# Performance work log

Measured on AMD Instinct MI355X. Metric: run time of the kernel, lower is better.

## Reference

```python
import jax, jax.numpy as jnp
import numpy as np

N_HEAD = 12

def setup_inputs() -> dict:
    key = jax.random.key(0)
    k1, k2, k3 = jax.random.split(key, 3)
    B, T, C = 8, 1024, 768
    x = jax.random.normal(k1, (B, T, C), dtype=jnp.float32)
    # torch Linear(768, 3*768): store as [in, out] so we can do x @ W
    W_attn = jax.random.normal(k2, (C, 3 * C), dtype=jnp.float32) * 0.02
    b_attn = jax.random.normal(k3, (3 * C,), dtype=jnp.float32) * 0.02
    return {"x": x, "W_attn": W_attn, "b_attn": b_attn}

def reference(x, W_attn, b_attn):
    B, T, C = x.shape
    H = N_HEAD
    hs = C // H
    scale = 1.0 / jnp.sqrt(jnp.asarray(hs, dtype=x.dtype))
    qkv = x @ W_attn + b_attn                      # [B,T,3C]
    q, k, v = jnp.split(qkv, 3, axis=-1)
    q = q.reshape(B, T, H, hs).transpose(0, 2, 1, 3)  # [B,H,T,hs]
    k = k.reshape(B, T, H, hs).transpose(0, 2, 1, 3)
    v = v.reshape(B, T, H, hs).transpose(0, 2, 1, 3)
    scores = jnp.einsum('bhqd,bhkd->bhqk', q, k) * scale
    # causal mask then ReLU (masked -inf entries become 0 after ReLU)
    causal = jnp.tril(jnp.ones((T, T), dtype=bool))
    att = jnp.where(causal[None, None], jax.nn.relu(scores), jnp.zeros((), dtype=scores.dtype))
    out = jnp.einsum('bhqk,bhkd->bhqd', att, v)    # [B,H,T,hs]
    out = out.transpose(0, 2, 1, 3).reshape(B, T, C)
    return out
```

## Files before the change

kernel.cpp:

```cpp
#include <hip/hip_runtime.h>

typedef __attribute__((ext_vector_type(8))) short bf16x8;
typedef __attribute__((ext_vector_type(4))) short bf16x4;
typedef __attribute__((ext_vector_type(4))) float f32x4;
typedef __attribute__((ext_vector_type(4))) unsigned short us4;
typedef __attribute__((ext_vector_type(8))) unsigned short us8;

#define MFMA(a, b, c) __builtin_amdgcn_mfma_f32_16x16x32_bf16((a), (b), (c), 0, 0, 0)
#define MFMA16(a, b, c) __builtin_amdgcn_mfma_f32_16x16x16bf16_1k((a), (b), (c), 0, 0, 0)

__device__ __forceinline__ unsigned short f2bf(float f) {
  unsigned u = __builtin_bit_cast(unsigned, f);
  u = (u + 0x7fffu + ((u >> 16) & 1u)) >> 16;
  return (unsigned short)u;
}

__device__ __forceinline__ unsigned cvt_pk_bf16(float lo, float hi) {
  unsigned r;
  asm("v_cvt_pk_bf16_f32 %0, %1, %2" : "=v"(r) : "v"(lo), "v"(hi));
  return r;
}

__device__ __forceinline__ void gload16(const void* g, void* l) {
  __builtin_amdgcn_global_load_lds((const __attribute__((address_space(1))) void*)g,
                                   (__attribute__((address_space(3))) void*)l,
                                   16, 0, 0);
}

__device__ __forceinline__ bf16x8 readfrag(const unsigned short* buf, int row, int kbyte) {
  int byte = row * 128 + kbyte;
  byte ^= (row & 7) << 4;
  return *(const bf16x8*)((const char*)buf + byte);
}

__device__ __forceinline__ bf16x4 readfrag64(const unsigned short* buf, int row, int col) {
  int byte = (row * 128 + col * 2) ^ ((row & 7) << 4);
  return *(const bf16x4*)((const char*)buf + byte);
}

__global__ void cast_x_kernel(const float* __restrict__ x,
                              unsigned short* __restrict__ xb, int n4) {
  int id = blockIdx.x * blockDim.x + threadIdx.x;
  if (id >= n4) return;
  float4 v = ((const float4*)x)[id];
  us4 o = { f2bf(v.x), f2bf(v.y), f2bf(v.z), f2bf(v.w) };
  ((us4*)xb)[id] = o;
}

__global__ void castw_kernel(const float* __restrict__ W,
                             unsigned short* __restrict__ Wt) {
  __shared__ unsigned short tile[32][33];
  int bn = blockIdx.x * 32;
  int bk = blockIdx.y * 32;
  int lx = threadIdx.x & 31, ly = threadIdx.x >> 5;
#pragma unroll
  for (int i = 0; i < 32; i += 8)
    tile[ly + i][lx] = f2bf(W[(bk + ly + i) * 2304 + bn + lx]);
  __syncthreads();
#pragma unroll
  for (int i = 0; i < 32; i += 8)
    Wt[(bn + ly + i) * 768 + bk + lx] = tile[lx][ly + i];
}

__global__ __launch_bounds__(256, 2) void qkv_gemm_kernel(
    const unsigned short* __restrict__ xb, const unsigned short* __restrict__ wt,
    const float* __restrict__ bias,
    unsigned short* __restrict__ qb, unsigned short* __restrict__ kb,
    unsigned short* __restrict__ vb) {
  __shared__ unsigned short lds[40960];
  const int tid = threadIdx.x;
  const int lane = tid & 63, wid = tid >> 6;
  const int wm = wid >> 1, wn = wid & 1;
  const int l15 = lane & 15, lg = lane >> 4;

  int bid = blockIdx.x;
  int xcd = bid & 7, c = bid >> 3;
  int mb = xcd * 8 + (c & 7);
  int nb = c >> 3;
  const int m0 = mb * 128, n0 = nb * 128;

  const unsigned short* Ab_g = xb + (size_t)m0 * 768;
  const unsigned short* Bb_g = wt + (size_t)n0 * 768;

  int eA[4], sA[4];
#pragma unroll
  for (int i = 0; i < 4; ++i) {
    int e = (i * 256 + tid) * 8, row = e >> 6;
    eA[i] = e;
    sA[i] = row * 768 + ((e ^ ((row & 7) << 3)) & 63);
  }

#define SA(buf, k0, i) gload16(Ab_g + sA[i] + (k0), &lds[(buf) * 8192 + eA[i]])
#define SB(buf, k0, i) gload16(Bb_g + sA[i] + (k0), &lds[24576 + (buf) * 8192 + eA[i]])

  f32x4 acc[4][4] = {};
  bf16x8 bfr[4][2];

  SA(0, 0, 0); SA(0, 0, 1); SA(0, 0, 2); SA(0, 0, 3);
  SB(0, 0, 0); SB(0, 0, 1); SB(0, 0, 2); SB(0, 0, 3);
  SA(1, 64, 0); SA(1, 64, 1); SA(1, 64, 2); SA(1, 64, 3);
  asm volatile("s_waitcnt vmcnt(4)" ::: "memory");
  __builtin_amdgcn_s_barrier();

#define GPHASE(cA_, cB_, P, STG, EW)                                              \
  {                                                                               \
    const unsigned short* Abuf = &lds[(cA_) * 8192];                              \
    const unsigned short* Bbuf = &lds[24576 + (cB_) * 8192];                      \
    bf16x8 afr[2][2];                                                             \
    _Pragma("unroll") for (int m2 = 0; m2 < 2; ++m2)                              \
        _Pragma("unroll") for (int kk = 0; kk < 2; ++kk)                          \
            afr[m2][kk] =                                                         \
        readfrag(Abuf, wm * 64 + ((P) * 2 + m2) * 16 + l15, kk * 64 + lg * 16);   \
    if ((P) == 0) {                                                               \
      _Pragma("unroll") for (int nf = 0; nf < 4; ++nf)                            \
          _Pragma("unroll") for (int kk = 0; kk < 2; ++kk)                        \
              bfr[nf][kk] =                                                       \
          readfrag(Bbuf, wn * 64 + nf * 16 + l15, kk * 64 + lg * 16);             \
    }                                                                             \
    STG;                                                                          \
    __builtin_amdgcn_sched_barrier(0);                                            \
    __builtin_amdgcn_s_barrier();                                                 \
    asm volatile("s_waitcnt lgkmcnt(0)" ::: "memory");                            \
    __builtin_amdgcn_sched_barrier(0);                                            \
    __builtin_amdgcn_s_setprio(1);                                                \
    _Pragma("unroll") for (int m2 = 0; m2 < 2; ++m2)                              \
        _Pragma("unroll") for (int nf = 0; nf < 4; ++nf)                          \
            _Pragma("unroll") for (int kk = 0; kk < 2; ++kk)                      \
                acc[(P) * 2 + m2][nf] =                                           \
        MFMA(afr[m2][kk], bfr[nf][kk], acc[(P) * 2 + m2][nf]);                    \
    __builtin_amdgcn_s_setprio(0);                                                \
    EW;                                                                           \
    __builtin_amdgcn_sched_barrier(0);                                            \
    __builtin_amdgcn_s_barrier();                                                 \
  }

  int cA = 0;
  for (int t = 0; t < 10; ++t) {
    int cB = t & 1, cBn = cB ^ 1;
    int cA2 = cA + 2; if (cA2 >= 3) cA2 -= 3;
    int k1 = (t + 1) * 64, k2 = (t + 2) * 64;
    GPHASE(cA, cB, 0, { SB(cBn, k1, 0); SB(cBn, k1, 1); SB(cBn, k1, 2); SB(cBn, k1, 3); }, );
    GPHASE(cA, cB, 1, { SA(cA2, k2, 0); SA(cA2, k2, 1); SA(cA2, k2, 2); SA(cA2, k2, 3); },
           asm volatile("s_waitcnt vmcnt(4)" ::: "memory"));
    cA = (cA == 2) ? 0 : cA + 1;
  }
  GPHASE(cA, 0, 0, { SB(1, 704, 0); SB(1, 704, 1); SB(1, 704, 2); SB(1, 704, 3); }, );
  GPHASE(cA, 0, 1, , asm volatile("s_waitcnt vmcnt(0)" ::: "memory"));
  cA = (cA == 2) ? 0 : cA + 1;
  GPHASE(cA, 1, 0, , );
  GPHASE(cA, 1, 1, , );

  __syncthreads();

  const int sec = n0 / 768;
  const float qscale = (sec == 0) ? 0.125f : 1.0f;
  float bcol[4];
#pragma unroll
  for (int nf = 0; nf < 4; ++nf) bcol[nf] = bias[n0 + wn * 64 + nf * 16 + l15];

  if (sec < 2) {
    unsigned short* ct = lds;
#pragma unroll
    for (int mf = 0; mf < 4; ++mf)
#pragma unroll
      for (int nf = 0; nf < 4; ++nf)
#pragma unroll
        for (int r = 0; r < 4; ++r)
          ct[(wm * 64 + mf * 16 + lg * 4 + r) * 128 + wn * 64 + nf * 16 + l15] =
              f2bf((acc[mf][nf][r] + bcol[nf]) * qscale);
    __syncthreads();
    unsigned short* dstbase = (sec == 0) ? qb : kb;
    const int hbase = (n0 - sec * 768) >> 6;
    const int g8 = tid >> 3, l8 = tid & 7;
#pragma unroll
    for (int j = 0; j < 8; ++j) {
      int chunk = j * 32 + g8;
      int row = chunk >> 1, hh = chunk & 1;
      us8 v = *(const us8*)&ct[row * 128 + hh * 64 + l8 * 8];
      int t = m0 + row, bb = t >> 10, tt = t & 1023;
      *(us8*)(dstbase + ((size_t)((bb * 12 + hbase + hh) * 1024 + tt)) * 64 + l8 * 8) = v;
    }
  } else {
#pragma unroll
    for (int nf = 0; nf < 4; ++nf) {
      int cc2 = (n0 - 1536) + wn * 64 + nf * 16 + l15;
      int h = cc2 >> 6, d = cc2 & 63;
#pragma unroll
      for (int mf = 0; mf < 4; ++mf) {
        int row0 = m0 + wm * 64 + mf * 16 + lg * 4;
        int bb = row0 >> 10, t0 = row0 & 1023;
        us4 o;
#pragma unroll
        for (int r = 0; r < 4; ++r) o[r] = f2bf(acc[mf][nf][r] + bcol[nf]);
        *(us4*)(vb + ((size_t)((bb * 12 + h) * 64 + d)) * 1024 + t0) = o;
      }
    }
  }
#undef SA
#undef SB
#undef GPHASE
}

__global__ __launch_bounds__(512, 2) void attn_kernel(
    const unsigned short* __restrict__ qb, const unsigned short* __restrict__ kb,
    const unsigned short* __restrict__ vb, float* __restrict__ out) {
  __shared__ unsigned short lds[32768];
  const int tid = threadIdx.x;
  const int lane = tid & 63, wid = tid >> 6;
  const int qs = wid >> 1, ks = wid & 1;
  const int l15 = lane & 15, lg = lane >> 4;

  int bid = blockIdx.x;
  int xcd = bid & 7, c = bid >> 3;
  int bh = xcd * 12 + (c % 12);
  int byq = 3 - (c / 12);
  const int b = bh / 12, h = bh % 12;
  const size_t base = (size_t)bh * 65536;
  const int Q = byq * 4 + qs;
  const int qr0 = byq * 256 + qs * 64;

  bf16x8 aq[4][2];
#pragma unroll
  for (int mf = 0; mf < 4; ++mf)
#pragma unroll
    for (int kk = 0; kk < 2; ++kk)
      aq[mf][kk] = *(const bf16x8*)(qb + base + (size_t)(qr0 + mf * 16 + l15) * 64 +
                                    kk * 32 + lg * 8);

  const int e = tid * 8;
  const int row = e >> 6;
  const int esw = e ^ ((row & 7) << 3);

#define ASTAGE(buf, i_)                                                            \
  {                                                                                \
    int kt0 = 2 * (i_);                                                            \
    gload16(kb + base + (size_t)kt0 * 4096 + esw, &lds[(buf) * 8192 + e]);         \
    gload16(kb + base + (size_t)(kt0 + 1) * 4096 + esw,                            \
            &lds[(buf) * 8192 + 4096 + e]);                                        \
    gload16(vb + base + (size_t)row * 1024 + kt0 * 64 + (esw & 63),                \
            &lds[16384 + (buf) * 8192 + e]);                                       \
    gload16(vb + base + (size_t)row * 1024 + (kt0 + 1) * 64 + (esw & 63),          \
            &lds[16384 + (buf) * 8192 + 4096 + e]);                                \
  }

  f32x4 o[4][4] = {};

  const int niter = 2 * byq + 2;
  ASTAGE(0, 0);
  asm volatile("s_waitcnt vmcnt(0)" ::: "memory");
  __builtin_amdgcn_s_barrier();

  for (int i = 0; i < niter; ++i) {
    const int cur = i & 1;
    if (i + 1 < niter) ASTAGE(cur ^ 1, i + 1);
    const int kt = 2 * i + ks;
    if (kt <= Q) {
      const unsigned short* Kb = &lds[cur * 8192 + ks * 4096];
      const unsigned short* Vb = &lds[16384 + cur * 8192 + ks * 4096];
      bf16x8 bk[4][2];
#pragma unroll
      for (int nf = 0; nf < 4; ++nf)
#pragma unroll
        for (int kk = 0; kk < 2; ++kk)
          bk[nf][kk] = readfrag(Kb, nf * 16 + l15, kk * 64 + lg * 16);
      bf16x4 vf[4][4];
#pragma unroll
      for (int nf = 0; nf < 4; ++nf)
#pragma unroll
        for (int df = 0; df < 4; ++df)
          vf[nf][df] = readfrag64(Vb, df * 16 + l15, nf * 16 + lg * 4);
      const bool diag = (kt == Q);
      bf16x4 pa[4][4];
      __builtin_amdgcn_s_setprio(1);
#pragma unroll
      for (int mf = 0; mf < 4; ++mf)
#pragma unroll
        for (int nf = 0; nf < 4; ++nf) {
          f32x4 s = {};
          s = MFMA(bk[nf][0], aq[mf][0], s);
          s = MFMA(bk[nf][1], aq[mf][1], s);
          float v0, v1, v2, v3;
          if (diag) {
            int q = mf * 16 + l15, k0 = nf * 16 + lg * 4;
            v0 = (k0 + 0 <= q) ? fmaxf(s[0], 0.0f) : 0.0f;
            v1 = (k0 + 1 <= q) ? fmaxf(s[1], 0.0f) : 0.0f;
            v2 = (k0 + 2 <= q) ? fmaxf(s[2], 0.0f) : 0.0f;
            v3 = (k0 + 3 <= q) ? fmaxf(s[3], 0.0f) : 0.0f;
          } else {
            v0 = fmaxf(s[0], 0.0f);
            v1 = fmaxf(s[1], 0.0f);
            v2 = fmaxf(s[2], 0.0f);
            v3 = fmaxf(s[3], 0.0f);
          }
          uint2 w;
          w.x = cvt_pk_bf16(v0, v1);
          w.y = cvt_pk_bf16(v2, v3);
          pa[mf][nf] = __builtin_bit_cast(bf16x4, w);
        }
#pragma unroll
      for (int nf = 0; nf < 4; ++nf)
#pragma unroll
        for (int mf = 0; mf < 4; ++mf)
#pragma unroll
          for (int df = 0; df < 4; ++df)
            o[mf][df] = MFMA16(pa[mf][nf], vf[nf][df], o[mf][df]);
      __builtin_amdgcn_s_setprio(0);
    }
    asm volatile("s_waitcnt vmcnt(0)" ::: "memory");
    __builtin_amdgcn_sched_barrier(0);
    __builtin_amdgcn_s_barrier();
  }
#undef ASTAGE

  float* fr = (float*)lds;
  if (ks == 1) {
#pragma unroll
    for (int mf = 0; mf < 4; ++mf)
#pragma unroll
      for (int df = 0; df < 4; ++df)
#pragma unroll
        for (int r = 0; r < 4; ++r) {
          int rowq = mf * 16 + lg * 4 + r, col = df * 16 + l15;
          int idx = (qs * 4096 + rowq * 64 + col) ^ ((rowq & 4) << 2);
          fr[idx] = o[mf][df][r];
        }
  }
  __syncthreads();
  if (ks == 0) {
#pragma unroll
    for (int mf = 0; mf < 4; ++mf)
#pragma unroll
      for (int df = 0; df < 4; ++df)
#pragma unroll
        for (int r = 0; r < 4; ++r) {
          int rowq = mf * 16 + lg * 4 + r, col = df * 16 + l15;
          int idx = (qs * 4096 + rowq * 64 + col) ^ ((rowq & 4) << 2);
          float v = o[mf][df][r] + fr[idx];
          out[(size_t)(b * 1024 + qr0 + rowq) * 768 + h * 64 + col] = v;
        }
  }
}

extern "C" void kernel_launch(void* const* d_in, const int* in_sizes, int n_in,
                              void* d_out, int out_size, void* d_ws, size_t ws_size,
                              hipStream_t stream) {
  const float* x = (const float*)d_in[0];
  const float* W = (const float*)d_in[1];
  const float* bias = (const float*)d_in[2];
  float* out = (float*)d_out;

  unsigned short* xb = (unsigned short*)d_ws;
  unsigned short* wt = xb + 6291456;
  unsigned short* qb = wt + 1769472;
  unsigned short* kb = qb + 6291456;
  unsigned short* vb = kb + 6291456;

  cast_x_kernel<<<6144, 256, 0, stream>>>(x, xb, 1572864);
  castw_kernel<<<dim3(72, 24), 256, 0, stream>>>(W, wt);
  qkv_gemm_kernel<<<1152, 256, 0, stream>>>(xb, wt, bias, qb, kb, vb);
  attn_kernel<<<384, 512, 0, stream>>>(qb, kb, vb, out);
}
```

Baseline: 84.63 us.

## Replace pipelined QKV GEMM with single-buffered loop and higher occupancy

```diff
diff --git a/kernel.cpp b/kernel.cpp
--- a/kernel.cpp
+++ b/kernel.cpp
@@ -62,12 +62,12 @@
     Wt[(bn + ly + i) * 768 + bk + lx] = tile[lx][ly + i];
 }
 
-__global__ __launch_bounds__(256, 2) void qkv_gemm_kernel(
+__global__ __launch_bounds__(256, 4) void qkv_gemm_kernel(
     const unsigned short* __restrict__ xb, const unsigned short* __restrict__ wt,
     const float* __restrict__ bias,
     unsigned short* __restrict__ qb, unsigned short* __restrict__ kb,
     unsigned short* __restrict__ vb) {
-  __shared__ unsigned short lds[40960];
+  __shared__ unsigned short lds[16384];
   const int tid = threadIdx.x;
   const int lane = tid & 63, wid = tid >> 6;
   const int wm = wid >> 1, wn = wid & 1;
@@ -90,67 +90,38 @@
     sA[i] = row * 768 + ((e ^ ((row & 7) << 3)) & 63);
   }
 
-#define SA(buf, k0, i) gload16(Ab_g + sA[i] + (k0), &lds[(buf) * 8192 + eA[i]])
-#define SB(buf, k0, i) gload16(Bb_g + sA[i] + (k0), &lds[24576 + (buf) * 8192 + eA[i]])
-
   f32x4 acc[4][4] = {};
-  bf16x8 bfr[4][2];
-
-  SA(0, 0, 0); SA(0, 0, 1); SA(0, 0, 2); SA(0, 0, 3);
-  SB(0, 0, 0); SB(0, 0, 1); SB(0, 0, 2); SB(0, 0, 3);
-  SA(1, 64, 0); SA(1, 64, 1); SA(1, 64, 2); SA(1, 64, 3);
-  asm volatile("s_waitcnt vmcnt(4)" ::: "memory");
-  __builtin_amdgcn_s_barrier();
-
-#define GPHASE(cA_, cB_, P, STG, EW)                                              \
-  {                                                                               \
-    const unsigned short* Abuf = &lds[(cA_) * 8192];                              \
-    const unsigned short* Bbuf = &lds[24576 + (cB_) * 8192];                      \
-    bf16x8 afr[2][2];                                                             \
-    _Pragma("unroll") for (int m2 = 0; m2 < 2; ++m2)                              \
-        _Pragma("unroll") for (int kk = 0; kk < 2; ++kk)                          \
-            afr[m2][kk] =                                                         \
-        readfrag(Abuf, wm * 64 + ((P) * 2 + m2) * 16 + l15, kk * 64 + lg * 16);   \
-    if ((P) == 0) {                                                               \
-      _Pragma("unroll") for (int nf = 0; nf < 4; ++nf)                            \
-          _Pragma("unroll") for (int kk = 0; kk < 2; ++kk)                        \
-              bfr[nf][kk] =                                                       \
-          readfrag(Bbuf, wn * 64 + nf * 16 + l15, kk * 64 + lg * 16);             \
-    }                                                                             \
-    STG;                                                                          \
-    __builtin_amdgcn_sched_barrier(0);                                            \
-    __builtin_amdgcn_s_barrier();                                                 \
-    asm volatile("s_waitcnt lgkmcnt(0)" ::: "memory");                            \
-    __builtin_amdgcn_sched_barrier(0);                                            \
-    __builtin_amdgcn_s_setprio(1);                                                \
-    _Pragma("unroll") for (int m2 = 0; m2 < 2; ++m2)                              \
-        _Pragma("unroll") for (int nf = 0; nf < 4; ++nf)                          \
-            _Pragma("unroll") for (int kk = 0; kk < 2; ++kk)                      \
-                acc[(P) * 2 + m2][nf] =                                           \
-        MFMA(afr[m2][kk], bfr[nf][kk], acc[(P) * 2 + m2][nf]);                    \
-    __builtin_amdgcn_s_setprio(0);                                                \
-    EW;                                                                           \
-    __builtin_amdgcn_sched_barrier(0);                                            \
-    __builtin_amdgcn_s_barrier();                                                 \
-  }
-
-  int cA = 0;
-  for (int t = 0; t < 10; ++t) {
-    int cB = t & 1, cBn = cB ^ 1;
-    int cA2 = cA + 2; if (cA2 >= 3) cA2 -= 3;
-    int k1 = (t + 1) * 64, k2 = (t + 2) * 64;
-    GPHASE(cA, cB, 0, { SB(cBn, k1, 0); SB(cBn, k1, 1); SB(cBn, k1, 2); SB(cBn, k1, 3); }, );
-    GPHASE(cA, cB, 1, { SA(cA2, k2, 0); SA(cA2, k2, 1); SA(cA2, k2, 2); SA(cA2, k2, 3); },
-           asm volatile("s_waitcnt vmcnt(4)" ::: "memory"));
-    cA = (cA == 2) ? 0 : cA + 1;
-  }
-  GPHASE(cA, 0, 0, { SB(1, 704, 0); SB(1, 704, 1); SB(1, 704, 2); SB(1, 704, 3); }, );
-  GPHASE(cA, 0, 1, , asm volatile("s_waitcnt vmcnt(0)" ::: "memory"));
-  cA = (cA == 2) ? 0 : cA + 1;
-  GPHASE(cA, 1, 0, , );
-  GPHASE(cA, 1, 1, , );
-
-  __syncthreads();
+
+  for (int t = 0; t < 12; ++t) {
+    const int k0 = t * 64;
+#pragma unroll
+    for (int i = 0; i < 4; ++i) {
+      gload16(Ab_g + sA[i] + k0, &lds[eA[i]]);
+      gload16(Bb_g + sA[i] + k0, &lds[8192 + eA[i]]);
+    }
+    asm volatile("s_waitcnt vmcnt(0)" ::: "memory");
+    __syncthreads();
+
+    bf16x8 afr[4][2], bfr[4][2];
+#pragma unroll
+    for (int mf = 0; mf < 4; ++mf)
+#pragma unroll
+      for (int kk = 0; kk < 2; ++kk)
+        afr[mf][kk] = readfrag(lds, wm * 64 + mf * 16 + l15, kk * 64 + lg * 16);
+#pragma unroll
+    for (int nf = 0; nf < 4; ++nf)
+#pragma unroll
+      for (int kk = 0; kk < 2; ++kk)
+        bfr[nf][kk] = readfrag(&lds[8192], wn * 64 + nf * 16 + l15, kk * 64 + lg * 16);
+#pragma unroll
+    for (int mf = 0; mf < 4; ++mf)
+#pragma unroll
+      for (int nf = 0; nf < 4; ++nf)
+#pragma unroll
+        for (int kk = 0; kk < 2; ++kk)
+          acc[mf][nf] = MFMA(afr[mf][kk], bfr[nf][kk], acc[mf][nf]);
+    __syncthreads();
+  }
 
   const int sec = n0 / 768;
   const float qscale = (sec == 0) ? 0.125f : 1.0f;
@@ -196,9 +167,6 @@
       }
     }
   }
-#undef SA
-#undef SB
-#undef GPHASE
 }
 
 __global__ __launch_bounds__(512, 2) void attn_kernel(
```

Result: slower. 87.76 us (+3.7%).

## Merge two-phase GEMM k-step into single iteration with one barrier

Applied to the files above, without the earlier changes.

```diff
diff --git a/kernel.cpp b/kernel.cpp
--- a/kernel.cpp
+++ b/kernel.cpp
@@ -94,7 +94,6 @@
 #define SB(buf, k0, i) gload16(Bb_g + sA[i] + (k0), &lds[24576 + (buf) * 8192 + eA[i]])
 
   f32x4 acc[4][4] = {};
-  bf16x8 bfr[4][2];
 
   SA(0, 0, 0); SA(0, 0, 1); SA(0, 0, 2); SA(0, 0, 3);
   SB(0, 0, 0); SB(0, 0, 1); SB(0, 0, 2); SB(0, 0, 3);
@@ -102,35 +101,27 @@
   asm volatile("s_waitcnt vmcnt(4)" ::: "memory");
   __builtin_amdgcn_s_barrier();
 
-#define GPHASE(cA_, cB_, P, STG, EW)                                              \
+#define GITER(cA_, cB_, STG, EW)                                                  \
   {                                                                               \
     const unsigned short* Abuf = &lds[(cA_) * 8192];                              \
     const unsigned short* Bbuf = &lds[24576 + (cB_) * 8192];                      \
-    bf16x8 afr[2][2];                                                             \
-    _Pragma("unroll") for (int m2 = 0; m2 < 2; ++m2)                              \
+    bf16x8 afr[4][2], bfr[4][2];                                                  \
+    _Pragma("unroll") for (int mf = 0; mf < 4; ++mf)                              \
         _Pragma("unroll") for (int kk = 0; kk < 2; ++kk)                          \
-            afr[m2][kk] =                                                         \
-        readfrag(Abuf, wm * 64 + ((P) * 2 + m2) * 16 + l15, kk * 64 + lg * 16);   \
-    if ((P) == 0) {                                                               \
-      _Pragma("unroll") for (int nf = 0; nf < 4; ++nf)                            \
-          _Pragma("unroll") for (int kk = 0; kk < 2; ++kk)                        \
-              bfr[nf][kk] =                                                       \
-          readfrag(Bbuf, wn * 64 + nf * 16 + l15, kk * 64 + lg * 16);             \
-    }                                                                             \
+            afr[mf][kk] =                                                         \
+        readfrag(Abuf, wm * 64 + mf * 16 + l15, kk * 64 + lg * 16);               \
+    _Pragma("unroll") for (int nf = 0; nf < 4; ++nf)                              \
+        _Pragma("unroll") for (int kk = 0; kk < 2; ++kk)                          \
+            bfr[nf][kk] =                                                         \
+        readfrag(Bbuf, wn * 64 + nf * 16 + l15, kk * 64 + lg * 16);               \
     STG;                                                                          \
-    __builtin_amdgcn_sched_barrier(0);                                            \
-    __builtin_amdgcn_s_barrier();                                                 \
-    asm volatile("s_waitcnt lgkmcnt(0)" ::: "memory");                            \
-    __builtin_amdgcn_sched_barrier(0);                                            \
     __builtin_amdgcn_s_setprio(1);                                                \
-    _Pragma("unroll") for (int m2 = 0; m2 < 2; ++m2)                              \
+    _Pragma("unroll") for (int mf = 0; mf < 4; ++mf)                              \
         _Pragma("unroll") for (int nf = 0; nf < 4; ++nf)                          \
             _Pragma("unroll") for (int kk = 0; kk < 2; ++kk)                      \
-                acc[(P) * 2 + m2][nf] =                                           \
-        MFMA(afr[m2][kk], bfr[nf][kk], acc[(P) * 2 + m2][nf]);                    \
+                acc[mf][nf] = MFMA(afr[mf][kk], bfr[nf][kk], acc[mf][nf]);        \
     __builtin_amdgcn_s_setprio(0);                                                \
     EW;                                                                           \
-    __builtin_amdgcn_sched_barrier(0);                                            \
     __builtin_amdgcn_s_barrier();                                                 \
   }
 
@@ -139,16 +130,16 @@
     int cB = t & 1, cBn = cB ^ 1;
     int cA2 = cA + 2; if (cA2 >= 3) cA2 -= 3;
     int k1 = (t + 1) * 64, k2 = (t + 2) * 64;
-    GPHASE(cA, cB, 0, { SB(cBn, k1, 0); SB(cBn, k1, 1); SB(cBn, k1, 2); SB(cBn, k1, 3); }, );
-    GPHASE(cA, cB, 1, { SA(cA2, k2, 0); SA(cA2, k2, 1); SA(cA2, k2, 2); SA(cA2, k2, 3); },
-           asm volatile("s_waitcnt vmcnt(4)" ::: "memory"));
+    GITER(cA, cB,
+          { SB(cBn, k1, 0); SB(cBn, k1, 1); SB(cBn, k1, 2); SB(cBn, k1, 3);
+            SA(cA2, k2, 0); SA(cA2, k2, 1); SA(cA2, k2, 2); SA(cA2, k2, 3); },
+          asm volatile("s_waitcnt vmcnt(4)" ::: "memory"));
     cA = (cA == 2) ? 0 : cA + 1;
   }
-  GPHASE(cA, 0, 0, { SB(1, 704, 0); SB(1, 704, 1); SB(1, 704, 2); SB(1, 704, 3); }, );
-  GPHASE(cA, 0, 1, , asm volatile("s_waitcnt vmcnt(0)" ::: "memory"));
+  GITER(cA, 0, { SB(1, 704, 0); SB(1, 704, 1); SB(1, 704, 2); SB(1, 704, 3); },
+        asm volatile("s_waitcnt vmcnt(0)" ::: "memory"));
   cA = (cA == 2) ? 0 : cA + 1;
-  GPHASE(cA, 1, 0, , );
-  GPHASE(cA, 1, 1, , );
+  GITER(cA, 1, , );
 
   __syncthreads();
 
@@ -198,7 +189,7 @@
   }
 #undef SA
 #undef SB
-#undef GPHASE
+#undef GITER
 }
 
 __global__ __launch_bounds__(512, 2) void attn_kernel(
```

Result: no change. 84.66 us (+0.0%).
